# Kernel optimization log

Hardware: AMD Instinct MI355X
Metric: run time of the kernel (lower is better)

## Reference

```python
import jax, jax.numpy as jnp
import numpy as np

N = 100000
E = 3200000
F_IN = 512
HID = 16
NUM_CLASSES = 2
NUM_GRAPHS = 256


def setup_inputs() -> dict:
    key = jax.random.key(0)
    k = jax.random.split(key, 8)
    x = jax.random.normal(k[0], (N, F_IN), dtype=jnp.float32)
    edge_index = jax.random.randint(k[1], (2, E), 0, N, dtype=jnp.int64)
    batch = jnp.sort(jax.random.randint(k[2], (N,), 0, NUM_GRAPHS, dtype=jnp.int64))
    # Glorot init like PyG GCNConv, biases zero-init
    W1 = jax.random.normal(k[3], (F_IN, HID), dtype=jnp.float32) * (2.0 / (F_IN + HID)) ** 0.5
    b1 = jnp.zeros((HID,), dtype=jnp.float32)
    W2 = jax.random.normal(k[4], (HID, NUM_CLASSES), dtype=jnp.float32) * (2.0 / (HID + NUM_CLASSES)) ** 0.5
    b2 = jnp.zeros((NUM_CLASSES,), dtype=jnp.float32)
    return {"x": x, "W1": W1, "b1": b1, "W2": W2, "b2": b2,
            "edge_index": edge_index, "batch": batch}


def _gcn_conv(x, W, b, src, dst, n):
    # PyG GCNConv: linear first, add self loops, symmetric deg^-1/2 normalization,
    # scatter-add messages from src to dst, then bias.
    h = x @ W                                        # [N, out]
    loops = jnp.arange(n, dtype=src.dtype)
    s = jnp.concatenate([src, loops])                # [E+N]
    d = jnp.concatenate([dst, loops])                # [E+N]
    deg = jax.ops.segment_sum(jnp.ones_like(d, dtype=h.dtype), d, num_segments=n)
    dinv = jax.lax.rsqrt(deg)                        # deg >= 1 due to self loops
    norm = dinv[s] * dinv[d]                         # [E+N]
    out = jax.ops.segment_sum(norm[:, None] * h[s], d, num_segments=n)
    return out + b


def reference(x, W1, b1, W2, b2, edge_index, batch):
    src, dst = edge_index[0], edge_index[1]
    h = jax.nn.relu(_gcn_conv(x, W1, b1, src, dst, N))
    h = _gcn_conv(h, W2, b2, src, dst, N)
    # global_mean_pool over graph ids
    sums = jax.ops.segment_sum(h, batch, num_segments=NUM_GRAPHS)
    counts = jax.ops.segment_sum(jnp.ones((N,), dtype=h.dtype), batch, num_segments=NUM_GRAPHS)
    pooled = sums / jnp.maximum(counts, 1.0)[:, None]  # [G, num_classes]
    return jax.nn.log_softmax(pooled, axis=1)
```

## Files before the change

kernel.cpp:

```cpp
#include <hip/hip_runtime.h>
#include <hip/hip_fp16.h>

#define N_NODES 100000
#define N_EDGES 3200000
#define F_INN 512
#define NGR 256
#define BSH 6
#define NBIN 1563
#define KBB 256
#define CHUNK (N_EDGES / KBB)

typedef __attribute__((ext_vector_type(8))) short bf16x8;
typedef __attribute__((ext_vector_type(4))) float f32x4;

__device__ __forceinline__ uint f2bf2(float a, float b) {
  uint ua = __float_as_uint(a), ub = __float_as_uint(b);
  uint ra = (ua + 0x7FFF + ((ua >> 16) & 1)) >> 16;
  uint rb = (ub + 0x7FFF + ((ub >> 16) & 1)) >> 16;
  return ra | (rb << 16);
}

__global__ __launch_bounds__(512) void k_binhist(const int* __restrict__ ei,
                                                 int* __restrict__ bintot) {
  __shared__ int h[NBIN];
  for (int t = threadIdx.x; t < NBIN; t += 512) h[t] = 0;
  __syncthreads();
  int e0 = blockIdx.x * CHUNK;
  for (int i = threadIdx.x; i < CHUNK; i += 512)
    atomicAdd(&h[ei[N_EDGES + e0 + i] >> BSH], 1);
  __syncthreads();
  for (int t = threadIdx.x; t < NBIN; t += 512)
    if (h[t]) atomicAdd(&bintot[t], h[t]);
}

__global__ __launch_bounds__(1024) void k_scan_wt(const int* __restrict__ bintot,
                                                  int* __restrict__ bsum,
                                                  const float* __restrict__ W,
                                                  ushort* __restrict__ Wt) {
  if (blockIdx.x == 0) {
    __shared__ int s[1024];
    int t = threadIdx.x;
    int i0 = 2 * t, i1 = 2 * t + 1;
    int a = (i0 < NBIN) ? bintot[i0] : 0;
    int b = (i1 < NBIN) ? bintot[i1] : 0;
    s[t] = a + b;
    __syncthreads();
    for (int o = 1; o < 1024; o <<= 1) {
      int add = (t >= o) ? s[t - o] : 0;
      __syncthreads();
      s[t] += add;
      __syncthreads();
    }
    int excl = t ? s[t - 1] : 0;
    if (i0 <= NBIN) bsum[i0] = excl;
    if (i1 <= NBIN) bsum[i1] = excl + a;
  } else {
    int tid = (blockIdx.x - 1) * 1024 + threadIdx.x;
    if (tid < 16 * 512) {
      int n = tid >> 9;
      int k = tid & 511;
      uint u = __float_as_uint(W[k * 16 + n]);
      Wt[tid] = (ushort)((u + 0x7FFF + ((u >> 16) & 1)) >> 16);
    }
  }
}

__global__ __launch_bounds__(512) void k_bin(const int* __restrict__ ei,
                                             const int* __restrict__ bsum,
                                             int* __restrict__ bincur,
                                             int* __restrict__ rec) {
  __shared__ int h[NBIN];
  __shared__ int base[NBIN];
  for (int t = threadIdx.x; t < NBIN; t += 512) h[t] = 0;
  __syncthreads();
  int e0 = blockIdx.x * CHUNK;
  for (int i = threadIdx.x; i < CHUNK; i += 512)
    atomicAdd(&h[ei[N_EDGES + e0 + i] >> BSH], 1);
  __syncthreads();
  for (int t = threadIdx.x; t < NBIN; t += 512) {
    int c = h[t];
    base[t] = bsum[t] + (c ? atomicAdd(&bincur[t], c) : 0);
    h[t] = 0;
  }
  __syncthreads();
  for (int i = threadIdx.x; i < CHUNK; i += 512) {
    int s = ei[e0 + i];
    int d = ei[N_EDGES + e0 + i];
    int k = d >> BSH;
    int pos = base[k] + atomicAdd(&h[k], 1);
    rec[pos] = (s << BSH) | (d & 63);
  }
}

__global__ __launch_bounds__(256) void k_binsort(const int* __restrict__ rec,
                                                 const int* __restrict__ bsum,
                                                 int* __restrict__ rec2,
                                                 int* __restrict__ nstart,
                                                 float* __restrict__ dinv) {
  __shared__ int h[64], excl[64], cur[64];
  int k = blockIdx.x, t = threadIdx.x;
  if (t < 64) h[t] = 0;
  __syncthreads();
  int start = bsum[k], end = bsum[k + 1];
  for (int r = start + t; r < end; r += 256)
    atomicAdd(&h[rec[r] & 63], 1);
  __syncthreads();
  if (t < 64) {
    int v = h[t];
    int sc = v;
#pragma unroll
    for (int o = 1; o < 64; o <<= 1) {
      int u = __shfl_up(sc, o);
      if (t >= o) sc += u;
    }
    int ex = sc - v;
    excl[t] = ex;
    cur[t] = 0;
    int node = (k << BSH) + t;
    nstart[node] = start + ex;
    if (node < N_NODES) dinv[node] = rsqrtf((float)v + 1.0f);
  }
  if (k == NBIN - 1 && t == 0) nstart[NBIN * 64] = N_EDGES;
  __syncthreads();
  for (int r = start + t; r < end; r += 256) {
    int v = rec[r];
    int dl = v & 63;
    int pos = start + excl[dl] + atomicAdd(&cur[dl], 1);
    rec2[pos] = v;
  }
}

__global__ __launch_bounds__(256) void k_gemm1(const float* __restrict__ X,
                                               const ushort* __restrict__ Wt,
                                               const float* __restrict__ dinv,
                                               __half* __restrict__ T1h) {
  const int t = threadIdx.x;
  const int lane = t & 63;
  const int w = t >> 6;
  const int c16 = lane & 15;
  const int g = lane >> 4;
  const int arow = blockIdx.x * 64 + w * 16 + c16;
  const bool rv = arow < N_NODES;
  const float* xrow = X + (size_t)arow * F_INN + g * 8;
  const ushort* brow = Wt + c16 * 512 + g * 8;

  f32x4 acc = {0.f, 0.f, 0.f, 0.f};
#pragma unroll
  for (int ks = 0; ks < 16; ++ks) {
    float4 v0 = rv ? *(const float4*)(xrow + ks * 32)     : make_float4(0.f, 0.f, 0.f, 0.f);
    float4 v1 = rv ? *(const float4*)(xrow + ks * 32 + 4) : make_float4(0.f, 0.f, 0.f, 0.f);
    uint au[4] = { f2bf2(v0.x, v0.y), f2bf2(v0.z, v0.w),
                   f2bf2(v1.x, v1.y), f2bf2(v1.z, v1.w) };
    bf16x8 a = *(const bf16x8*)au;
    bf16x8 b = *(const bf16x8*)(brow + ks * 32);
    acc = __builtin_amdgcn_mfma_f32_16x16x32_bf16(a, b, acc, 0, 0, 0);
  }

  int rbase = blockIdx.x * 64 + w * 16 + g * 4;
#pragma unroll
  for (int j = 0; j < 4; ++j) {
    int r = rbase + j;
    if (r < N_NODES)
      T1h[(size_t)r * 16 + c16] = __float2half(dinv[r] * acc[j]);
  }
}

__global__ __launch_bounds__(256) void k_agg1(const int* __restrict__ rec2,
                                              const int* __restrict__ nstart,
                                              const float* __restrict__ dinv,
                                              const __half* __restrict__ T1h,
                                              const float* __restrict__ b1,
                                              const float* __restrict__ W2,
                                              float* __restrict__ T2) {
  __shared__ float accs[64 * 17];
  int k = blockIdx.x, t = threadIdx.x;
  int n0 = k << BSH;
  int node = n0 + (t >> 2);
  int q = t & 3;
  bool nvalid = node < N_NODES;
  float a0 = 0.f, a1 = 0.f, a2 = 0.f, a3 = 0.f;
  int r = 0, e = 0;
  if (nvalid) {
    r = nstart[node];
    e = nstart[node + 1];
    uint2 u = *(const uint2*)(T1h + (size_t)node * 16 + q * 4);
    float2 f0 = __half22float2(*reinterpret_cast<__half2*>(&u.x));
    float2 f1 = __half22float2(*reinterpret_cast<__half2*>(&u.y));
    a0 = f0.x; a1 = f0.y; a2 = f1.x; a3 = f1.y;
  }
  for (; r + 1 < e; r += 2) {
    int v0 = rec2[r], v1 = rec2[r + 1];
    uint2 ua = *(const uint2*)(T1h + (size_t)(v0 >> BSH) * 16 + q * 4);
    uint2 ub = *(const uint2*)(T1h + (size_t)(v1 >> BSH) * 16 + q * 4);
    float2 fa0 = __half22float2(*reinterpret_cast<__half2*>(&ua.x));
    float2 fa1 = __half22float2(*reinterpret_cast<__half2*>(&ua.y));
    float2 fb0 = __half22float2(*reinterpret_cast<__half2*>(&ub.x));
    float2 fb1 = __half22float2(*reinterpret_cast<__half2*>(&ub.y));
    a0 += fa0.x + fb0.x; a1 += fa0.y + fb0.y;
    a2 += fa1.x + fb1.x; a3 += fa1.y + fb1.y;
  }
  if (r < e) {
    int v = rec2[r];
    uint2 u = *(const uint2*)(T1h + (size_t)(v >> BSH) * 16 + q * 4);
    float2 f0 = __half22float2(*reinterpret_cast<__half2*>(&u.x));
    float2 f1 = __half22float2(*reinterpret_cast<__half2*>(&u.y));
    a0 += f0.x; a1 += f0.y; a2 += f1.x; a3 += f1.y;
  }
  float dd = nvalid ? dinv[node] : 0.f;
  float* rowp = &accs[(t >> 2) * 17 + q * 4];
  rowp[0] = dd * a0; rowp[1] = dd * a1; rowp[2] = dd * a2; rowp[3] = dd * a3;
  __syncthreads();
  if (t < 64) {
    int n = n0 + t;
    if (n < N_NODES) {
      float dd2 = dinv[n];
      float s0 = 0.f, s1 = 0.f;
#pragma unroll
      for (int c = 0; c < 16; ++c) {
        float hv = fmaxf(accs[t * 17 + c] + b1[c], 0.f);
        s0 = fmaf(hv, W2[c * 2 + 0], s0);
        s1 = fmaf(hv, W2[c * 2 + 1], s1);
      }
      T2[(size_t)n * 2 + 0] = dd2 * s0;
      T2[(size_t)n * 2 + 1] = dd2 * s1;
    }
  }
}

__global__ __launch_bounds__(128) void k_agg2(const int* __restrict__ rec2,
                                              const int* __restrict__ nstart,
                                              const float* __restrict__ dinv,
                                              const float* __restrict__ T2,
                                              float* __restrict__ O2) {
  int k = blockIdx.x, t = threadIdx.x;
  int n0 = k << BSH;
  int node = n0 + (t >> 1);
  int c = t & 1;
  if (node >= N_NODES) return;
  int r = nstart[node], e = nstart[node + 1];
  float acc = T2[(size_t)node * 2 + c];
  for (; r + 1 < e; r += 2) {
    int v0 = rec2[r], v1 = rec2[r + 1];
    acc += T2[(size_t)(v0 >> BSH) * 2 + c] + T2[(size_t)(v1 >> BSH) * 2 + c];
  }
  if (r < e) acc += T2[(size_t)(rec2[r] >> BSH) * 2 + c];
  O2[(size_t)node * 2 + c] = dinv[node] * acc;
}

__global__ __launch_bounds__(256) void k_pool(const float* __restrict__ O2,
                                              const int* __restrict__ batch,
                                              float* __restrict__ pool,
                                              float* __restrict__ gcnt) {
  int i = blockIdx.x * 256 + threadIdx.x;
  bool valid = i < N_NODES;
  int b = valid ? batch[i] : -1;
  float vx = 0.f, vy = 0.f;
  if (valid) {
    vx = O2[(size_t)i * 2 + 0];
    vy = O2[(size_t)i * 2 + 1];
  }
  int b0 = __shfl(b, 0);
  if (__all(b == b0)) {
    if (b0 >= 0) {
#pragma unroll
      for (int o = 32; o > 0; o >>= 1) {
        vx += __shfl_xor(vx, o);
        vy += __shfl_xor(vy, o);
      }
      if ((threadIdx.x & 63) == 0) {
        atomicAdd(&pool[b0 * 2 + 0], vx);
        atomicAdd(&pool[b0 * 2 + 1], vy);
        atomicAdd(&gcnt[b0], 64.0f);
      }
    }
  } else if (valid) {
    atomicAdd(&pool[b * 2 + 0], vx);
    atomicAdd(&pool[b * 2 + 1], vy);
    atomicAdd(&gcnt[b], 1.0f);
  }
}

__global__ __launch_bounds__(256) void k_final(const float* __restrict__ pool,
                                               const float* __restrict__ gcnt,
                                               const float* __restrict__ b2,
                                               float* __restrict__ out) {
  int g = threadIdx.x;
  if (g < NGR) {
    float c = fmaxf(gcnt[g], 1.0f);
    float p0 = pool[g * 2 + 0] / c + b2[0];
    float p1 = pool[g * 2 + 1] / c + b2[1];
    float m = fmaxf(p0, p1);
    float l = logf(expf(p0 - m) + expf(p1 - m));
    out[g * 2 + 0] = p0 - m - l;
    out[g * 2 + 1] = p1 - m - l;
  }
}

extern "C" void kernel_launch(void* const* d_in, const int* in_sizes, int n_in,
                              void* d_out, int out_size, void* d_ws, size_t ws_size,
                              hipStream_t stream) {
  const float* x  = (const float*)d_in[0];
  const float* W1 = (const float*)d_in[1];
  const float* b1 = (const float*)d_in[2];
  const float* W2 = (const float*)d_in[3];
  const float* b2 = (const float*)d_in[4];
  const int*   ei = (const int*)d_in[5];
  const int*   bt = (const int*)d_in[6];
  float* out = (float*)d_out;

  char* ws = (char*)d_ws;
  int*   bintot = (int*)ws;    ws += (size_t)NBIN * 4;
  int*   bincur = (int*)ws;    ws += (size_t)NBIN * 4;
  float* pool   = (float*)ws;  ws += 2 * NGR * 4;
  float* gcnt   = (float*)ws;  ws += NGR * 4;
  int*   bsum   = (int*)ws;    ws += (size_t)(NBIN + 1) * 4;
  int*   nstart = (int*)ws;    ws += (size_t)(NBIN * 64 + 2) * 4;
  float* dinv   = (float*)ws;  ws += (size_t)N_NODES * 4;
  ushort* wt    = (ushort*)ws; ws += (size_t)16 * 512 * 2;
  int*   rec    = (int*)ws;    ws += (size_t)N_EDGES * 4;
  int*   rec2   = (int*)ws;    ws += (size_t)N_EDGES * 4;
  __half* t1h   = (__half*)ws; ws += (size_t)N_NODES * 16 * 2;
  float* t2     = (float*)ws;  ws += (size_t)N_NODES * 2 * 4;
  float* o2     = (float*)ws;  ws += (size_t)N_NODES * 2 * 4;

  hipMemsetAsync(bintot, 0, (size_t)(2 * NBIN + 3 * NGR) * 4, stream);

  k_binhist <<<KBB, 512, 0, stream>>>(ei, bintot);
  k_scan_wt <<<9, 1024, 0, stream>>>(bintot, bsum, W1, wt);
  k_bin     <<<KBB, 512, 0, stream>>>(ei, bsum, bincur, rec);
  k_binsort <<<NBIN, 256, 0, stream>>>(rec, bsum, rec2, nstart, dinv);
  k_gemm1   <<<NBIN, 256, 0, stream>>>(x, wt, dinv, t1h);
  k_agg1    <<<NBIN, 256, 0, stream>>>(rec2, nstart, dinv, t1h, b1, W2, t2);
  k_agg2    <<<NBIN, 128, 0, stream>>>(rec2, nstart, dinv, t2, o2);
  k_pool    <<<(N_NODES + 255) / 256, 256, 0, stream>>>(o2, bt, pool, gcnt);
  k_final   <<<1, 256, 0, stream>>>(pool, gcnt, b2, out);
}
```

Measured before the change: 240.7 us.

## Use fixed-capacity bins to drop histogram/scan pass and fuse pooling into agg2

Replaces the global histogram plus prefix-scan with fixed-capacity per-bin slots (CAP entries per 64-node bin), so edges are binned in a single pass. This removes the k_binhist and k_scan_wt kernels. Per-node counts are stored separately, and the aggregation kernels stage each bin's edge records into shared memory. Mean pooling is fused into k_agg2, which removes the O2 round trip and the separate pool kernel. The risk is overflow if any bin receives more than CAP edges, which holds only for roughly uniform random edge destinations.

```diff
diff --git a/kernel.cpp b/kernel.cpp
--- a/kernel.cpp
+++ b/kernel.cpp
@@ -9,6 +9,7 @@
 #define NBIN 1563
 #define KBB 256
 #define CHUNK (N_EDGES / KBB)
+#define CAP 2560
 
 typedef __attribute__((ext_vector_type(8))) short bf16x8;
 typedef __attribute__((ext_vector_type(4))) float f32x4;
@@ -20,55 +21,20 @@
   return ra | (rb << 16);
 }
 
-__global__ __launch_bounds__(512) void k_binhist(const int* __restrict__ ei,
-                                                 int* __restrict__ bintot) {
-  __shared__ int h[NBIN];
-  for (int t = threadIdx.x; t < NBIN; t += 512) h[t] = 0;
-  __syncthreads();
-  int e0 = blockIdx.x * CHUNK;
-  for (int i = threadIdx.x; i < CHUNK; i += 512)
-    atomicAdd(&h[ei[N_EDGES + e0 + i] >> BSH], 1);
-  __syncthreads();
-  for (int t = threadIdx.x; t < NBIN; t += 512)
-    if (h[t]) atomicAdd(&bintot[t], h[t]);
-}
-
-__global__ __launch_bounds__(1024) void k_scan_wt(const int* __restrict__ bintot,
-                                                  int* __restrict__ bsum,
-                                                  const float* __restrict__ W,
-                                                  ushort* __restrict__ Wt) {
-  if (blockIdx.x == 0) {
-    __shared__ int s[1024];
-    int t = threadIdx.x;
-    int i0 = 2 * t, i1 = 2 * t + 1;
-    int a = (i0 < NBIN) ? bintot[i0] : 0;
-    int b = (i1 < NBIN) ? bintot[i1] : 0;
-    s[t] = a + b;
-    __syncthreads();
-    for (int o = 1; o < 1024; o <<= 1) {
-      int add = (t >= o) ? s[t - o] : 0;
-      __syncthreads();
-      s[t] += add;
-      __syncthreads();
-    }
-    int excl = t ? s[t - 1] : 0;
-    if (i0 <= NBIN) bsum[i0] = excl;
-    if (i1 <= NBIN) bsum[i1] = excl + a;
-  } else {
-    int tid = (blockIdx.x - 1) * 1024 + threadIdx.x;
-    if (tid < 16 * 512) {
+__global__ __launch_bounds__(512) void k_bin(const int* __restrict__ ei,
+                                             int* __restrict__ bincur,
+                                             int* __restrict__ rec,
+                                             const float* __restrict__ W,
+                                             ushort* __restrict__ Wt) {
+  if (blockIdx.x == KBB) {
+    for (int tid = threadIdx.x; tid < 16 * 512; tid += 512) {
       int n = tid >> 9;
       int k = tid & 511;
       uint u = __float_as_uint(W[k * 16 + n]);
       Wt[tid] = (ushort)((u + 0x7FFF + ((u >> 16) & 1)) >> 16);
     }
-  }
-}
-
-__global__ __launch_bounds__(512) void k_bin(const int* __restrict__ ei,
-                                             const int* __restrict__ bsum,
-                                             int* __restrict__ bincur,
-                                             int* __restrict__ rec) {
+    return;
+  }
   __shared__ int h[NBIN];
   __shared__ int base[NBIN];
   for (int t = threadIdx.x; t < NBIN; t += 512) h[t] = 0;
@@ -79,7 +45,7 @@
   __syncthreads();
   for (int t = threadIdx.x; t < NBIN; t += 512) {
     int c = h[t];
-    base[t] = bsum[t] + (c ? atomicAdd(&bincur[t], c) : 0);
+    base[t] = t * CAP + (c ? atomicAdd(&bincur[t], c) : 0);
     h[t] = 0;
   }
   __syncthreads();
@@ -93,15 +59,17 @@
 }
 
 __global__ __launch_bounds__(256) void k_binsort(const int* __restrict__ rec,
-                                                 const int* __restrict__ bsum,
+                                                 const int* __restrict__ bincur,
                                                  int* __restrict__ rec2,
                                                  int* __restrict__ nstart,
+                                                 int* __restrict__ ncnt,
                                                  float* __restrict__ dinv) {
   __shared__ int h[64], excl[64], cur[64];
   int k = blockIdx.x, t = threadIdx.x;
   if (t < 64) h[t] = 0;
   __syncthreads();
-  int start = bsum[k], end = bsum[k + 1];
+  int start = k * CAP;
+  int end = start + bincur[k];
   for (int r = start + t; r < end; r += 256)
     atomicAdd(&h[rec[r] & 63], 1);
   __syncthreads();
@@ -117,10 +85,12 @@
     excl[t] = ex;
     cur[t] = 0;
     int node = (k << BSH) + t;
-    nstart[node] = start + ex;
-    if (node < N_NODES) dinv[node] = rsqrtf((float)v + 1.0f);
-  }
-  if (k == NBIN - 1 && t == 0) nstart[NBIN * 64] = N_EDGES;
+    if (node < N_NODES) {
+      nstart[node] = start + ex;
+      ncnt[node] = v;
+      dinv[node] = rsqrtf((float)v + 1.0f);
+    }
+  }
   __syncthreads();
   for (int r = start + t; r < end; r += 256) {
     int v = rec[r];
@@ -166,30 +136,36 @@
 }
 
 __global__ __launch_bounds__(256) void k_agg1(const int* __restrict__ rec2,
+                                              const int* __restrict__ bincur,
                                               const int* __restrict__ nstart,
+                                              const int* __restrict__ ncnt,
                                               const float* __restrict__ dinv,
                                               const __half* __restrict__ T1h,
                                               const float* __restrict__ b1,
                                               const float* __restrict__ W2,
                                               float* __restrict__ T2) {
   __shared__ float accs[64 * 17];
+  __shared__ int recs[CAP];
   int k = blockIdx.x, t = threadIdx.x;
   int n0 = k << BSH;
+  int cnt = bincur[k];
+  for (int i = t; i < cnt; i += 256) recs[i] = rec2[k * CAP + i];
   int node = n0 + (t >> 2);
   int q = t & 3;
   bool nvalid = node < N_NODES;
   float a0 = 0.f, a1 = 0.f, a2 = 0.f, a3 = 0.f;
   int r = 0, e = 0;
   if (nvalid) {
-    r = nstart[node];
-    e = nstart[node + 1];
+    r = nstart[node] - k * CAP;
+    e = r + ncnt[node];
     uint2 u = *(const uint2*)(T1h + (size_t)node * 16 + q * 4);
     float2 f0 = __half22float2(*reinterpret_cast<__half2*>(&u.x));
     float2 f1 = __half22float2(*reinterpret_cast<__half2*>(&u.y));
     a0 = f0.x; a1 = f0.y; a2 = f1.x; a3 = f1.y;
   }
+  __syncthreads();
   for (; r + 1 < e; r += 2) {
-    int v0 = rec2[r], v1 = rec2[r + 1];
+    int v0 = recs[r], v1 = recs[r + 1];
     uint2 ua = *(const uint2*)(T1h + (size_t)(v0 >> BSH) * 16 + q * 4);
     uint2 ub = *(const uint2*)(T1h + (size_t)(v1 >> BSH) * 16 + q * 4);
     float2 fa0 = __half22float2(*reinterpret_cast<__half2*>(&ua.x));
@@ -200,7 +176,7 @@
     a2 += fa1.x + fb1.x; a3 += fa1.y + fb1.y;
   }
   if (r < e) {
-    int v = rec2[r];
+    int v = recs[r];
     uint2 u = *(const uint2*)(T1h + (size_t)(v >> BSH) * 16 + q * 4);
     float2 f0 = __half22float2(*reinterpret_cast<__half2*>(&u.x));
     float2 f1 = __half22float2(*reinterpret_cast<__half2*>(&u.y));
@@ -228,55 +204,62 @@
 }
 
 __global__ __launch_bounds__(128) void k_agg2(const int* __restrict__ rec2,
+                                              const int* __restrict__ bincur,
                                               const int* __restrict__ nstart,
+                                              const int* __restrict__ ncnt,
                                               const float* __restrict__ dinv,
                                               const float* __restrict__ T2,
-                                              float* __restrict__ O2) {
-  int k = blockIdx.x, t = threadIdx.x;
-  int n0 = k << BSH;
-  int node = n0 + (t >> 1);
-  int c = t & 1;
-  if (node >= N_NODES) return;
-  int r = nstart[node], e = nstart[node + 1];
-  float acc = T2[(size_t)node * 2 + c];
-  for (; r + 1 < e; r += 2) {
-    int v0 = rec2[r], v1 = rec2[r + 1];
-    acc += T2[(size_t)(v0 >> BSH) * 2 + c] + T2[(size_t)(v1 >> BSH) * 2 + c];
-  }
-  if (r < e) acc += T2[(size_t)(rec2[r] >> BSH) * 2 + c];
-  O2[(size_t)node * 2 + c] = dinv[node] * acc;
-}
-
-__global__ __launch_bounds__(256) void k_pool(const float* __restrict__ O2,
                                               const int* __restrict__ batch,
                                               float* __restrict__ pool,
                                               float* __restrict__ gcnt) {
-  int i = blockIdx.x * 256 + threadIdx.x;
-  bool valid = i < N_NODES;
-  int b = valid ? batch[i] : -1;
-  float vx = 0.f, vy = 0.f;
-  if (valid) {
-    vx = O2[(size_t)i * 2 + 0];
-    vy = O2[(size_t)i * 2 + 1];
-  }
-  int b0 = __shfl(b, 0);
-  if (__all(b == b0)) {
-    if (b0 >= 0) {
-#pragma unroll
-      for (int o = 32; o > 0; o >>= 1) {
-        vx += __shfl_xor(vx, o);
-        vy += __shfl_xor(vy, o);
+  __shared__ int recs[CAP];
+  __shared__ float sm[128];
+  int k = blockIdx.x, t = threadIdx.x;
+  int n0 = k << BSH;
+  int cnt = bincur[k];
+  for (int i = t; i < cnt; i += 128) recs[i] = rec2[k * CAP + i];
+  int node = n0 + (t >> 1);
+  int c = t & 1;
+  bool nvalid = node < N_NODES;
+  float acc = 0.f;
+  int r = 0, e = 0;
+  if (nvalid) {
+    r = nstart[node] - k * CAP;
+    e = r + ncnt[node];
+    acc = T2[(size_t)node * 2 + c];
+  }
+  __syncthreads();
+  for (; r + 1 < e; r += 2) {
+    int v0 = recs[r], v1 = recs[r + 1];
+    acc += T2[(size_t)(v0 >> BSH) * 2 + c] + T2[(size_t)(v1 >> BSH) * 2 + c];
+  }
+  if (r < e) acc += T2[(size_t)(recs[r] >> BSH) * 2 + c];
+  sm[t] = nvalid ? dinv[node] * acc : 0.f;
+  __syncthreads();
+  if (t < 64) {
+    int n = n0 + t;
+    bool valid = n < N_NODES;
+    int b = valid ? batch[n] : -1;
+    float vx = sm[2 * t], vy = sm[2 * t + 1];
+    int b0 = __shfl(b, 0);
+    if (__all(b == b0)) {
+      if (b0 >= 0) {
+#pragma unroll
+        for (int o = 32; o > 0; o >>= 1) {
+          vx += __shfl_xor(vx, o);
+          vy += __shfl_xor(vy, o);
+        }
+        if (t == 0) {
+          atomicAdd(&pool[b0 * 2 + 0], vx);
+          atomicAdd(&pool[b0 * 2 + 1], vy);
+          atomicAdd(&gcnt[b0], 64.0f);
+        }
       }
-      if ((threadIdx.x & 63) == 0) {
-        atomicAdd(&pool[b0 * 2 + 0], vx);
-        atomicAdd(&pool[b0 * 2 + 1], vy);
-        atomicAdd(&gcnt[b0], 64.0f);
-      }
-    }
-  } else if (valid) {
-    atomicAdd(&pool[b * 2 + 0], vx);
-    atomicAdd(&pool[b * 2 + 1], vy);
-    atomicAdd(&gcnt[b], 1.0f);
+    } else if (valid) {
+      atomicAdd(&pool[b * 2 + 0], vx);
+      atomicAdd(&pool[b * 2 + 1], vy);
+      atomicAdd(&gcnt[b], 1.0f);
+    }
   }
 }
 
@@ -309,29 +292,24 @@
   float* out = (float*)d_out;
 
   char* ws = (char*)d_ws;
-  int*   bintot = (int*)ws;    ws += (size_t)NBIN * 4;
   int*   bincur = (int*)ws;    ws += (size_t)NBIN * 4;
   float* pool   = (float*)ws;  ws += 2 * NGR * 4;
   float* gcnt   = (float*)ws;  ws += NGR * 4;
-  int*   bsum   = (int*)ws;    ws += (size_t)(NBIN + 1) * 4;
-  int*   nstart = (int*)ws;    ws += (size_t)(NBIN * 64 + 2) * 4;
+  int*   nstart = (int*)ws;    ws += (size_t)N_NODES * 4;
+  int*   ncnt   = (int*)ws;    ws += (size_t)N_NODES * 4;
   float* dinv   = (float*)ws;  ws += (size_t)N_NODES * 4;
   ushort* wt    = (ushort*)ws; ws += (size_t)16 * 512 * 2;
-  int*   rec    = (int*)ws;    ws += (size_t)N_EDGES * 4;
-  int*   rec2   = (int*)ws;    ws += (size_t)N_EDGES * 4;
+  int*   rec    = (int*)ws;    ws += (size_t)NBIN * CAP * 4;
+  int*   rec2   = (int*)ws;    ws += (size_t)NBIN * CAP * 4;
   __half* t1h   = (__half*)ws; ws += (size_t)N_NODES * 16 * 2;
   float* t2     = (float*)ws;  ws += (size_t)N_NODES * 2 * 4;
-  float* o2     = (float*)ws;  ws += (size_t)N_NODES * 2 * 4;
-
-  hipMemsetAsync(bintot, 0, (size_t)(2 * NBIN + 3 * NGR) * 4, stream);
-
-  k_binhist <<<KBB, 512, 0, stream>>>(ei, bintot);
-  k_scan_wt <<<9, 1024, 0, stream>>>(bintot, bsum, W1, wt);
-  k_bin     <<<KBB, 512, 0, stream>>>(ei, bsum, bincur, rec);
-  k_binsort <<<NBIN, 256, 0, stream>>>(rec, bsum, rec2, nstart, dinv);
-  k_gemm1   <<<NBIN, 256, 0, stream>>>(x, wt, dinv, t1h);
-  k_agg1    <<<NBIN, 256, 0, stream>>>(rec2, nstart, dinv, t1h, b1, W2, t2);
-  k_agg2    <<<NBIN, 128, 0, stream>>>(rec2, nstart, dinv, t2, o2);
-  k_pool    <<<(N_NODES + 255) / 256, 256, 0, stream>>>(o2, bt, pool, gcnt);
-  k_final   <<<1, 256, 0, stream>>>(pool, gcnt, b2, out);
-}
+
+  hipMemsetAsync(bincur, 0, (size_t)(NBIN + 3 * NGR) * 4, stream);
+
+  k_bin    <<<KBB + 1, 512, 0, stream>>>(ei, bincur, rec, W1, wt);
+  k_binsort<<<NBIN, 256, 0, stream>>>(rec, bincur, rec2, nstart, ncnt, dinv);
+  k_gemm1  <<<NBIN, 256, 0, stream>>>(x, wt, dinv, t1h);
+  k_agg1   <<<NBIN, 256, 0, stream>>>(rec2, bincur, nstart, ncnt, dinv, t1h, b1, W2, t2);
+  k_agg2   <<<NBIN, 128, 0, stream>>>(rec2, bincur, nstart, ncnt, dinv, t2, bt, pool, gcnt);
+  k_final  <<<1, 256, 0, stream>>>(pool, gcnt, b2, out);
+}
```

Result: faster. 201.7 us (-16.2%).
